# Kernel tuning notes

Hardware: AMD Instinct MI355X
Metric: run time of the kernel (lower is better)

## Reference

```python
import jax, jax.numpy as jnp
import numpy as np

GH, GW, H, B, IN = 4, 2, 512, 8192, 1
FC_HID = H // 2
NC = GH * GW
BN_EPS = 1e-5


def setup_inputs() -> dict:
    key = jax.random.key(0)
    ks = jax.random.split(key, 20)
    def n(k, shape, s=1.0):
        return jax.random.normal(k, shape, dtype=jnp.float32) * s
    return {
        "x": n(ks[0], (B, GH, GW)),
        "h_ext": n(ks[1], (B, H), 0.1),
        "c_ext": n(ks[2], (B, H), 0.1),
        "grid_h": n(ks[3], (GH, GW, B, H), 0.1),
        "grid_c": n(ks[4], (GH, GW, B, H), 0.1),
        "Wh": n(ks[5], (NC, H, 3 * H), (3 * H) ** -0.5),
        "bh": n(ks[6], (NC, H), 0.01),
        "Wc": n(ks[7], (NC, H, 3 * H), (3 * H) ** -0.5),
        "bc": n(ks[8], (NC, H), 0.01),
        "W_ih": n(ks[9], (NC, 4 * H, IN), 1.0),
        "W_hh": n(ks[10], (NC, 4 * H, H), H ** -0.5),
        "b_ih": n(ks[11], (NC, 4 * H), 0.01),
        "b_hh": n(ks[12], (NC, 4 * H), 0.01),
        "W1": n(ks[13], (FC_HID, 2 * H), (2 * H) ** -0.5),
        "b1": n(ks[14], (FC_HID,), 0.01),
        "W2": n(ks[15], (1, FC_HID), FC_HID ** -0.5),
        "b2": n(ks[16], (1,), 0.01),
        "gamma": jnp.ones((1,), jnp.float32),
        "beta": jnp.zeros((1,), jnp.float32),
    }


def _lattice_forward(x, h_ext, c_ext, grid_h, grid_c, Wh, bh, Wc, bc,
                     W_ih, W_hh, b_ih, b_hh, W1, b1, W2, b2, gamma, beta):
    b = x.shape[0]
    zeros = jnp.zeros((b, H), x.dtype)
    # python lists over the small fixed 4x2 grid (strict left/up dependency)
    sh = [[grid_h[i, j] for j in range(GW)] for i in range(GH)]
    sc = [[grid_c[i, j] for j in range(GW)] for i in range(GH)]
    for i in range(GH):
        for j in range(GW):
            k = i * GW + j
            h_prev, c_prev = sh[i][j], sc[i][j]
            if i == 0 and j == 0:
                h_left, c_left = h_ext, c_ext
            elif j > 0:
                h_left, c_left = sh[i][j - 1], sc[i][j - 1]
            else:
                h_left, c_left = zeros, zeros
            if i > 0:
                h_up, c_up = sh[i - 1][j], sc[i - 1][j]
            else:
                h_up, c_up = zeros, zeros
            comb_h = jnp.concatenate([h_left, h_up, h_prev], axis=1)  # [B,3H]
            comb_c = jnp.concatenate([c_left, c_up, c_prev], axis=1)
            ph = comb_h @ Wh[k].T + bh[k]  # [B,H]
            pc = comb_c @ Wc[k].T + bc[k]
            xi = x[:, i, j][:, None]  # [B,1]
            gates = xi @ W_ih[k].T + b_ih[k] + ph @ W_hh[k].T + b_hh[k]  # [B,4H]
            ig, fg, gg, og = jnp.split(gates, 4, axis=1)
            c_new = jax.nn.sigmoid(fg) * pc + jax.nn.sigmoid(ig) * jnp.tanh(gg)
            h_new = jax.nn.sigmoid(og) * jnp.tanh(c_new)
            sh[i][j], sc[i][j] = h_new, c_new
    final_h = sh[-1][-1] + h_ext
    final_c = sc[-1][-1] + c_ext
    final = jnp.concatenate([final_h, final_c], axis=1)  # [B,2H]
    hid = jax.nn.relu(final @ W1.T + b1)
    out = hid @ W2.T + b2  # [B,1]
    # BatchNorm1d in training mode: biased batch stats over the batch dim
    mu = jnp.mean(out, axis=0, keepdims=True)
    var = jnp.mean((out - mu) ** 2, axis=0, keepdims=True)
    out = gamma * (out - mu) * jax.lax.rsqrt(var + BN_EPS) + beta
    out = jax.nn.sigmoid(out)
    new_gh = jnp.stack([jnp.stack(row) for row in sh])  # [GH,GW,B,H]
    new_gc = jnp.stack([jnp.stack(row) for row in sc])
    return out, final_h, final_c, new_gh, new_gc


def reference(x, h_ext, c_ext, grid_h, grid_c, Wh, bh, Wc, bc,
              W_ih, W_hh, b_ih, b_hh, W1, b1, W2, b2, gamma, beta):
    return _lattice_forward(x, h_ext, c_ext, grid_h, grid_c, Wh, bh, Wc, bc,
                            W_ih, W_hh, b_ih, b_hh, W1, b1, W2, b2, gamma, beta)
```

## Files before the change

kernel.cpp:

```cpp
#include <hip/hip_runtime.h>
#include <stdint.h>

#define B_SZ 8192
#define H_SZ 512

typedef short bfrag8 __attribute__((ext_vector_type(8)));
typedef float f32x4 __attribute__((ext_vector_type(4)));

__device__ __forceinline__ unsigned short f2bf(float f) {
  union { float f; uint32_t u; } c; c.f = f;
  uint32_t u = c.u;
  uint32_t r = (u + 0x7FFFu + ((u >> 16) & 1u)) >> 16;
  return (unsigned short)r;
}
__device__ __forceinline__ float bf2f(unsigned short u) {
  union { uint32_t u; float f; } c; c.u = ((uint32_t)u) << 16;
  return c.f;
}
__device__ __forceinline__ float sigm(float x) { return 1.0f / (1.0f + __expf(-x)); }
__device__ __forceinline__ float tanh_fast(float x) {
  float cx = fminf(fmaxf(x, -15.0f), 15.0f);
  float e = __expf(2.0f * cx);
  return (e - 1.0f) / (e + 1.0f);
}

__device__ __forceinline__ void gload16(const void* g, void* l) {
  __builtin_amdgcn_global_load_lds(
      (const __attribute__((address_space(1))) void*)g,
      (__attribute__((address_space(3))) void*)l, 16, 0, 0);
}

struct GemmArgs {
  const unsigned short* Ah[3];
  const unsigned short* Ac[3];
  const unsigned short* Bh;
  const unsigned short* Bc;
  int ldA, ldB;
  const float* biash;
  const float* biasc;
  unsigned short* outBf;
  float* outF;
  const float* pc;
  const float* x;
  const float* W_ih;
  const float* b_ih;
  const float* b_hh;
  int cell, last;
  float* gh_out; float* gc_out;
  unsigned short* ring_h; unsigned short* ring_c;
  const float* h_ext; const float* c_ext;
  float* fh_out; float* fc_out;
  unsigned short* finalBf;
};

template <int MODE>
__global__ __launch_bounds__(256, 2)
void gemm_k(GemmArgs g) {
  __shared__ __align__(16) char As[16384];
  __shared__ __align__(16) char Bs[16384];
  const int tid = threadIdx.x;
  const int lane = tid & 63;
  const int wv = tid >> 6;
  const int wr = wv >> 1, wc = wv & 1;
  const int m0 = blockIdx.y * 128;
  const int z = (MODE == 0) ? blockIdx.z : 0;

  const unsigned short* const* Aseg = (MODE == 0 && z == 1) ? g.Ac : g.Ah;
  const unsigned short* Bb = (MODE == 0 && z == 1) ? g.Bc : g.Bh;

  int rowA[4], cgA[4];
  const char* browPtr[4];
#pragma unroll
  for (int q = 0; q < 4; ++q) {
    int cl = q * 256 + tid;
    int row = cl >> 3, cs = cl & 7;
    cgA[q] = cs ^ (row & 7);
    rowA[q] = row;
    int browG;
    if (MODE == 1) {
      int gate = (row >> 4) & 3;
      int hh = blockIdx.x * 32 + ((row >> 6) << 4) + (row & 15);
      browG = gate * 512 + hh;
    } else {
      browG = blockIdx.x * 128 + row;
    }
    browPtr[q] = (const char*)Bb + (size_t)browG * g.ldB * 2;
  }

  f32x4 acc[4][4];
#pragma unroll
  for (int a = 0; a < 4; ++a)
#pragma unroll
    for (int b = 0; b < 4; ++b) acc[a][b] = f32x4{0.f, 0.f, 0.f, 0.f};

  const int NSEG = (MODE == 1) ? 1 : ((MODE == 2) ? 2 : 3);
  for (int s = 0; s < NSEG; ++s) {
    const unsigned short* Ab = Aseg[s];
    if (MODE == 0 && Ab == 0) continue;
    const char* Abase = (const char*)Ab;
    const int kOffB = s * 1024;
    for (int k0 = 0; k0 < 512; k0 += 64) {
#pragma unroll
      for (int q = 0; q < 4; ++q)
        gload16(Abase + ((size_t)(m0 + rowA[q]) * g.ldA + k0) * 2 + cgA[q] * 16,
                As + (q * 256 + tid) * 16);
#pragma unroll
      for (int q = 0; q < 4; ++q)
        gload16(browPtr[q] + kOffB + k0 * 2 + cgA[q] * 16,
                Bs + (q * 256 + tid) * 16);
      __syncthreads();
#pragma unroll
      for (int ks = 0; ks < 2; ++ks) {
        bfrag8 af[4], bfr[4];
#pragma unroll
        for (int mf = 0; mf < 4; ++mf) {
          int row = wr * 64 + mf * 16 + (lane & 15);
          af[mf] = *(const bfrag8*)(As + row * 128 +
                                    ((ks * 4 + (lane >> 4)) ^ (row & 7)) * 16);
        }
#pragma unroll
        for (int nf = 0; nf < 4; ++nf) {
          int row = wc * 64 + nf * 16 + (lane & 15);
          bfr[nf] = *(const bfrag8*)(Bs + row * 128 +
                                     ((ks * 4 + (lane >> 4)) ^ (row & 7)) * 16);
        }
#pragma unroll
        for (int mf = 0; mf < 4; ++mf)
#pragma unroll
          for (int nf = 0; nf < 4; ++nf)
            acc[mf][nf] = __builtin_amdgcn_mfma_f32_16x16x32_bf16(
                af[mf], bfr[nf], acc[mf][nf], 0, 0, 0);
      }
      __syncthreads();
    }
  }

  const int c4 = lane & 15;
  const int r4 = lane >> 4;

  if (MODE == 0) {
    const float* bias = (z == 0) ? g.biash : g.biasc;
    const int n0 = blockIdx.x * 128;
#pragma unroll
    for (int nf = 0; nf < 4; ++nf) {
      int colg = n0 + wc * 64 + nf * 16 + c4;
      float bv = bias[colg];
#pragma unroll
      for (int mf = 0; mf < 4; ++mf)
#pragma unroll
        for (int r = 0; r < 4; ++r) {
          int rowg = m0 + wr * 64 + mf * 16 + r4 * 4 + r;
          float v = acc[mf][nf][r] + bv;
          if (z == 0) g.outBf[(size_t)rowg * 512 + colg] = f2bf(v);
          else        g.outF[(size_t)rowg * 512 + colg] = v;
        }
    }
  } else if (MODE == 2) {
    const int n0 = blockIdx.x * 128;
#pragma unroll
    for (int nf = 0; nf < 4; ++nf) {
      int colg = n0 + wc * 64 + nf * 16 + c4;
      float bv = g.biash[colg];
#pragma unroll
      for (int mf = 0; mf < 4; ++mf)
#pragma unroll
        for (int r = 0; r < 4; ++r) {
          int rowg = m0 + wr * 64 + mf * 16 + r4 * 4 + r;
          float v = fmaxf(acc[mf][nf][r] + bv, 0.0f);
          g.outBf[(size_t)rowg * 256 + colg] = f2bf(v);
        }
    }
  } else {
    int hcol = blockIdx.x * 32 + wc * 16 + c4;
    float wih[4], gb[4];
#pragma unroll
    for (int q = 0; q < 4; ++q) {
      wih[q] = g.W_ih[q * 512 + hcol];
      gb[q] = g.b_ih[q * 512 + hcol] + g.b_hh[q * 512 + hcol];
    }
#pragma unroll
    for (int mf = 0; mf < 4; ++mf)
#pragma unroll
      for (int r = 0; r < 4; ++r) {
        int b = m0 + wr * 64 + mf * 16 + r4 * 4 + r;
        float xi = g.x[b * 8 + g.cell];
        float vi = acc[mf][0][r] + xi * wih[0] + gb[0];
        float vf = acc[mf][1][r] + xi * wih[1] + gb[1];
        float vg = acc[mf][2][r] + xi * wih[2] + gb[2];
        float vo = acc[mf][3][r] + xi * wih[3] + gb[3];
        size_t offo = (size_t)b * 512 + hcol;
        float pcv = g.pc[offo];
        float cn = sigm(vf) * pcv + sigm(vi) * tanh_fast(vg);
        float hn = sigm(vo) * tanh_fast(cn);
        g.gh_out[offo] = hn;
        g.gc_out[offo] = cn;
        g.ring_h[offo] = f2bf(hn);
        g.ring_c[offo] = f2bf(cn);
        if (g.last) {
          float fh = hn + g.h_ext[offo];
          float fc = cn + g.c_ext[offo];
          g.fh_out[offo] = fh;
          g.fc_out[offo] = fc;
          g.finalBf[(size_t)b * 1024 + hcol] = f2bf(fh);
          g.finalBf[(size_t)b * 1024 + 512 + hcol] = f2bf(fc);
        }
      }
  }
}

__global__ __launch_bounds__(256)
void convert_pair(const float4* s0, uint2* d0, size_t n0,
                  const float4* s1, uint2* d1, size_t n1) {
  size_t total = n0 + n1;
  size_t stride = (size_t)gridDim.x * blockDim.x;
  for (size_t idx = (size_t)blockIdx.x * blockDim.x + threadIdx.x; idx < total;
       idx += stride) {
    const float4* s; uint2* d; size_t j;
    if (idx < n0) { s = s0; d = d0; j = idx; }
    else          { s = s1; d = d1; j = idx - n0; }
    float4 v = s[j];
    uint2 o;
    o.x = (uint32_t)f2bf(v.x) | ((uint32_t)f2bf(v.y) << 16);
    o.y = (uint32_t)f2bf(v.z) | ((uint32_t)f2bf(v.w) << 16);
    d[j] = o;
  }
}

__global__ __launch_bounds__(256)
void fc2_kernel(const unsigned short* hid, const float* W2, const float* b2,
                float* outlin) {
  int row = blockIdx.x * 4 + (threadIdx.x >> 6);
  int lane = threadIdx.x & 63;
  uint2 hv = ((const uint2*)(hid + (size_t)row * 256))[lane];
  float4 wv = ((const float4*)W2)[lane];
  float s = bf2f((unsigned short)(hv.x & 0xffffu)) * wv.x +
            bf2f((unsigned short)(hv.x >> 16)) * wv.y +
            bf2f((unsigned short)(hv.y & 0xffffu)) * wv.z +
            bf2f((unsigned short)(hv.y >> 16)) * wv.w;
#pragma unroll
  for (int o = 32; o > 0; o >>= 1) s += __shfl_down(s, o);
  if (lane == 0) outlin[row] = s + b2[0];
}

__global__ __launch_bounds__(1024)
void bn_kernel(const float* outlin, const float* gamma, const float* beta,
               float* out) {
  __shared__ float sred[16], sred2[16];
  __shared__ float smu, srs;
  float s = 0.f, s2 = 0.f;
  for (int i = threadIdx.x; i < 8192; i += 1024) {
    float v = outlin[i];
    s += v; s2 += v * v;
  }
#pragma unroll
  for (int o = 32; o > 0; o >>= 1) { s += __shfl_down(s, o); s2 += __shfl_down(s2, o); }
  if ((threadIdx.x & 63) == 0) { sred[threadIdx.x >> 6] = s; sred2[threadIdx.x >> 6] = s2; }
  __syncthreads();
  if (threadIdx.x == 0) {
    float S = 0.f, S2 = 0.f;
    for (int q = 0; q < 16; ++q) { S += sred[q]; S2 += sred2[q]; }
    float mu = S * (1.0f / 8192.0f);
    float var = S2 * (1.0f / 8192.0f) - mu * mu;
    smu = mu; srs = rsqrtf(var + 1e-5f);
  }
  __syncthreads();
  float gm = gamma[0], bt = beta[0];
  for (int i = threadIdx.x; i < 8192; i += 1024) {
    float v = (outlin[i] - smu) * srs * gm + bt;
    out[i] = sigm(v);
  }
}

extern "C" void kernel_launch(void* const* d_in, const int* in_sizes, int n_in,
                              void* d_out, int out_size, void* d_ws, size_t ws_size,
                              hipStream_t stream) {
  const float* x      = (const float*)d_in[0];
  const float* h_ext  = (const float*)d_in[1];
  const float* c_ext  = (const float*)d_in[2];
  const float* grid_h = (const float*)d_in[3];
  const float* grid_c = (const float*)d_in[4];
  const float* Wh     = (const float*)d_in[5];
  const float* bh     = (const float*)d_in[6];
  const float* Wc     = (const float*)d_in[7];
  const float* bc     = (const float*)d_in[8];
  const float* W_ih   = (const float*)d_in[9];
  const float* W_hh   = (const float*)d_in[10];
  const float* b_ih   = (const float*)d_in[11];
  const float* b_hh   = (const float*)d_in[12];
  const float* W1     = (const float*)d_in[13];
  const float* b1     = (const float*)d_in[14];
  const float* W2     = (const float*)d_in[15];
  const float* b2     = (const float*)d_in[16];
  const float* gamma  = (const float*)d_in[17];
  const float* beta   = (const float*)d_in[18];

  float* out = (float*)d_out;
  const size_t BH = (size_t)B_SZ * H_SZ;
  float* fh_out = out + 8192;
  float* fc_out = fh_out + BH;
  float* gh_out = fc_out + BH;
  float* gc_out = gh_out + 8 * BH;

  char* ws = (char*)d_ws;
  size_t off = 0;
  auto alloc = [&](size_t bytes) {
    char* p = ws + off;
    off = (off + bytes + 255) & ~(size_t)255;
    return p;
  };
  unsigned short* whB   = (unsigned short*)alloc(8ull * 512 * 1536 * 2);
  unsigned short* wcB   = (unsigned short*)alloc(8ull * 512 * 1536 * 2);
  unsigned short* whhB  = (unsigned short*)alloc(8ull * 2048 * 512 * 2);
  unsigned short* w1B   = (unsigned short*)alloc(256ull * 1024 * 2);
  unsigned short* hextB = (unsigned short*)alloc(BH * 2);
  unsigned short* cextB = (unsigned short*)alloc(BH * 2);
  unsigned short* ringH[3]; unsigned short* ringC[3];
  for (int s = 0; s < 3; ++s) {
    ringH[s] = (unsigned short*)alloc(BH * 2);
    ringC[s] = (unsigned short*)alloc(BH * 2);
  }
  unsigned short* phB    = (unsigned short*)alloc(BH * 2);
  float*          pcF    = (float*)alloc(BH * 4);
  unsigned short* finalB = (unsigned short*)alloc((size_t)B_SZ * 1024 * 2);
  unsigned short* hidB   = (unsigned short*)alloc((size_t)B_SZ * 256 * 2);
  float*          outlin = (float*)alloc((size_t)B_SZ * 4);

  convert_pair<<<2048, 256, 0, stream>>>((const float4*)Wh, (uint2*)whB, 8ull * 512 * 1536 / 4,
                                         (const float4*)Wc, (uint2*)wcB, 8ull * 512 * 1536 / 4);
  convert_pair<<<2048, 256, 0, stream>>>((const float4*)W_hh, (uint2*)whhB, 8ull * 2048 * 512 / 4,
                                         (const float4*)W1, (uint2*)w1B, 256ull * 1024 / 4);
  convert_pair<<<2048, 256, 0, stream>>>((const float4*)h_ext, (uint2*)hextB, BH / 4,
                                         (const float4*)c_ext, (uint2*)cextB, BH / 4);

  for (int cell = 0; cell < 8; ++cell) {
    int i = cell >> 1, j = cell & 1;
    int slot = cell % 3;
    convert_pair<<<2048, 256, 0, stream>>>(
        (const float4*)(grid_h + cell * BH), (uint2*)ringH[slot], BH / 4,
        (const float4*)(grid_c + cell * BH), (uint2*)ringC[slot], BH / 4);

    GemmArgs a = {};
    const unsigned short *hl, *cl_, *hu, *cu;
    if (cell == 0)      { hl = hextB;              cl_ = cextB; }
    else if (j > 0)     { hl = ringH[(cell - 1) % 3]; cl_ = ringC[(cell - 1) % 3]; }
    else                { hl = 0;                  cl_ = 0; }
    if (i > 0)          { hu = ringH[(cell - 2) % 3]; cu = ringC[(cell - 2) % 3]; }
    else                { hu = 0;                  cu = 0; }
    a.Ah[0] = hl; a.Ah[1] = hu; a.Ah[2] = ringH[slot];
    a.Ac[0] = cl_; a.Ac[1] = cu; a.Ac[2] = ringC[slot];
    a.Bh = whB + (size_t)cell * 512 * 1536;
    a.Bc = wcB + (size_t)cell * 512 * 1536;
    a.ldA = 512; a.ldB = 1536;
    a.biash = bh + cell * 512; a.biasc = bc + cell * 512;
    a.outBf = phB; a.outF = pcF;
    gemm_k<0><<<dim3(4, 64, 2), 256, 0, stream>>>(a);

    GemmArgs ga = {};
    ga.Ah[0] = phB; ga.ldA = 512;
    ga.Bh = whhB + (size_t)cell * 2048 * 512; ga.ldB = 512;
    ga.pc = pcF; ga.x = x;
    ga.W_ih = W_ih + cell * 2048;
    ga.b_ih = b_ih + cell * 2048;
    ga.b_hh = b_hh + cell * 2048;
    ga.cell = cell; ga.last = (cell == 7);
    ga.gh_out = gh_out + cell * BH; ga.gc_out = gc_out + cell * BH;
    ga.ring_h = ringH[slot]; ga.ring_c = ringC[slot];
    ga.h_ext = h_ext; ga.c_ext = c_ext;
    ga.fh_out = fh_out; ga.fc_out = fc_out; ga.finalBf = finalB;
    gemm_k<1><<<dim3(16, 64, 1), 256, 0, stream>>>(ga);
  }

  GemmArgs gf = {};
  gf.Ah[0] = finalB; gf.Ah[1] = finalB + 512; gf.ldA = 1024;
  gf.Bh = w1B; gf.ldB = 1024;
  gf.biash = b1;
  gf.outBf = hidB;
  gemm_k<2><<<dim3(2, 64, 1), 256, 0, stream>>>(gf);

  fc2_kernel<<<2048, 256, 0, stream>>>(hidB, W2, b2, outlin);
  bn_kernel<<<1, 1024, 0, stream>>>(outlin, gamma, beta, out);
}
```

Baseline: 786.0 us.

## Precompute h_prev/c_prev projections for all cells and batch lattice diagonals

```diff
diff --git a/kernel.cpp b/kernel.cpp
--- a/kernel.cpp
+++ b/kernel.cpp
@@ -3,6 +3,7 @@
 
 #define B_SZ 8192
 #define H_SZ 512
+static const size_t BH = (size_t)B_SZ * H_SZ;
 
 typedef short bfrag8 __attribute__((ext_vector_type(8)));
 typedef float f32x4 __attribute__((ext_vector_type(4)));
@@ -30,61 +31,40 @@
       (__attribute__((address_space(3))) void*)l, 16, 0, 0);
 }
 
-struct GemmArgs {
-  const unsigned short* Ah[3];
-  const unsigned short* Ac[3];
-  const unsigned short* Bh;
-  const unsigned short* Bc;
-  int ldA, ldB;
-  const float* biash;
-  const float* biasc;
+struct PJob {
+  const unsigned short* A0;
+  const unsigned short* A1;
+  int co0, co1, nseg, relu;
+  const unsigned short* B;
+  const float* bias;
+  const float* partial;
   unsigned short* outBf;
   float* outF;
-  const float* pc;
-  const float* x;
-  const float* W_ih;
-  const float* b_ih;
-  const float* b_hh;
-  int cell, last;
-  float* gh_out; float* gc_out;
-  unsigned short* ring_h; unsigned short* ring_c;
-  const float* h_ext; const float* c_ext;
-  float* fh_out; float* fc_out;
-  unsigned short* finalBf;
 };
-
-template <int MODE>
-__global__ __launch_bounds__(256, 2)
-void gemm_k(GemmArgs g) {
+struct PArgs {
+  PJob j[16];
+  int ldA, ldB, outStride;
+};
+
+__global__ __launch_bounds__(256, 2) void pgemm_k(PArgs pa) {
   __shared__ __align__(16) char As[16384];
   __shared__ __align__(16) char Bs[16384];
+  const PJob jb = pa.j[blockIdx.z];
   const int tid = threadIdx.x;
   const int lane = tid & 63;
   const int wv = tid >> 6;
   const int wr = wv >> 1, wc = wv & 1;
   const int m0 = blockIdx.y * 128;
-  const int z = (MODE == 0) ? blockIdx.z : 0;
-
-  const unsigned short* const* Aseg = (MODE == 0 && z == 1) ? g.Ac : g.Ah;
-  const unsigned short* Bb = (MODE == 0 && z == 1) ? g.Bc : g.Bh;
-
-  int rowA[4], cgA[4];
+
+  int rowA[4], cg[4];
   const char* browPtr[4];
 #pragma unroll
   for (int q = 0; q < 4; ++q) {
     int cl = q * 256 + tid;
     int row = cl >> 3, cs = cl & 7;
-    cgA[q] = cs ^ (row & 7);
+    cg[q] = cs ^ (row & 7);
     rowA[q] = row;
-    int browG;
-    if (MODE == 1) {
-      int gate = (row >> 4) & 3;
-      int hh = blockIdx.x * 32 + ((row >> 6) << 4) + (row & 15);
-      browG = gate * 512 + hh;
-    } else {
-      browG = blockIdx.x * 128 + row;
-    }
-    browPtr[q] = (const char*)Bb + (size_t)browG * g.ldB * 2;
+    browPtr[q] = (const char*)jb.B + (size_t)(blockIdx.x * 128 + row) * pa.ldB * 2;
   }
 
   f32x4 acc[4][4];
@@ -93,20 +73,17 @@
 #pragma unroll
     for (int b = 0; b < 4; ++b) acc[a][b] = f32x4{0.f, 0.f, 0.f, 0.f};
 
-  const int NSEG = (MODE == 1) ? 1 : ((MODE == 2) ? 2 : 3);
-  for (int s = 0; s < NSEG; ++s) {
-    const unsigned short* Ab = Aseg[s];
-    if (MODE == 0 && Ab == 0) continue;
-    const char* Abase = (const char*)Ab;
-    const int kOffB = s * 1024;
+  for (int s = 0; s < jb.nseg; ++s) {
+    const char* Abase = (const char*)(s ? jb.A1 : jb.A0);
+    const int coB = (s ? jb.co1 : jb.co0) * 2;
     for (int k0 = 0; k0 < 512; k0 += 64) {
 #pragma unroll
       for (int q = 0; q < 4; ++q)
-        gload16(Abase + ((size_t)(m0 + rowA[q]) * g.ldA + k0) * 2 + cgA[q] * 16,
+        gload16(Abase + ((size_t)(m0 + rowA[q]) * pa.ldA + k0) * 2 + cg[q] * 16,
                 As + (q * 256 + tid) * 16);
 #pragma unroll
       for (int q = 0; q < 4; ++q)
-        gload16(browPtr[q] + kOffB + k0 * 2 + cgA[q] * 16,
+        gload16(browPtr[q] + coB + k0 * 2 + cg[q] * 16,
                 Bs + (q * 256 + tid) * 16);
       __syncthreads();
 #pragma unroll
@@ -137,92 +114,166 @@
 
   const int c4 = lane & 15;
   const int r4 = lane >> 4;
-
-  if (MODE == 0) {
-    const float* bias = (z == 0) ? g.biash : g.biasc;
-    const int n0 = blockIdx.x * 128;
-#pragma unroll
-    for (int nf = 0; nf < 4; ++nf) {
-      int colg = n0 + wc * 64 + nf * 16 + c4;
-      float bv = bias[colg];
+  const int n0 = blockIdx.x * 128;
+#pragma unroll
+  for (int nf = 0; nf < 4; ++nf) {
+    int colg = n0 + wc * 64 + nf * 16 + c4;
+    float bv = jb.bias ? jb.bias[colg] : 0.0f;
+#pragma unroll
+    for (int mf = 0; mf < 4; ++mf)
+#pragma unroll
+      for (int r = 0; r < 4; ++r) {
+        int rowg = m0 + wr * 64 + mf * 16 + r4 * 4 + r;
+        size_t o = (size_t)rowg * pa.outStride + colg;
+        float v = acc[mf][nf][r] + bv;
+        if (jb.partial) v += jb.partial[o];
+        if (jb.relu) v = fmaxf(v, 0.0f);
+        if (jb.outBf) jb.outBf[o] = f2bf(v);
+        if (jb.outF) jb.outF[o] = v;
+      }
+  }
+}
+
+struct GJob {
+  const unsigned short* ph;
+  const unsigned short* Whh;
+  const float* pc;
+  float* gh; float* gc;
+  unsigned short* nh; unsigned short* nc;
+  int cell, last;
+};
+struct GArgs {
+  GJob j[2];
+  const float* x;
+  const float* W_ih; const float* b_ih; const float* b_hh;
+  const float* h_ext; const float* c_ext;
+  float* fh; float* fc;
+  unsigned short* finalB;
+};
+
+__global__ __launch_bounds__(256, 2) void gates_k(GArgs ga) {
+  __shared__ __align__(16) char As[16384];
+  __shared__ __align__(16) char Bs[16384];
+  const GJob jb = ga.j[blockIdx.z];
+  const int tid = threadIdx.x;
+  const int lane = tid & 63;
+  const int wv = tid >> 6;
+  const int wr = wv >> 1, wc = wv & 1;
+  const int m0 = blockIdx.y * 128;
+
+  int rowA[4], cg[4];
+  const char* browPtr[4];
+#pragma unroll
+  for (int q = 0; q < 4; ++q) {
+    int cl = q * 256 + tid;
+    int row = cl >> 3, cs = cl & 7;
+    cg[q] = cs ^ (row & 7);
+    rowA[q] = row;
+    int gate = (row >> 4) & 3;
+    int hh = blockIdx.x * 32 + ((row >> 6) << 4) + (row & 15);
+    browPtr[q] = (const char*)jb.Whh + (size_t)(gate * 512 + hh) * 512 * 2;
+  }
+
+  f32x4 acc[4][4];
+#pragma unroll
+  for (int a = 0; a < 4; ++a)
+#pragma unroll
+    for (int b = 0; b < 4; ++b) acc[a][b] = f32x4{0.f, 0.f, 0.f, 0.f};
+
+  for (int k0 = 0; k0 < 512; k0 += 64) {
+#pragma unroll
+    for (int q = 0; q < 4; ++q)
+      gload16((const char*)jb.ph + ((size_t)(m0 + rowA[q]) * 512 + k0) * 2 + cg[q] * 16,
+              As + (q * 256 + tid) * 16);
+#pragma unroll
+    for (int q = 0; q < 4; ++q)
+      gload16(browPtr[q] + k0 * 2 + cg[q] * 16, Bs + (q * 256 + tid) * 16);
+    __syncthreads();
+#pragma unroll
+    for (int ks = 0; ks < 2; ++ks) {
+      bfrag8 af[4], bfr[4];
+#pragma unroll
+      for (int mf = 0; mf < 4; ++mf) {
+        int row = wr * 64 + mf * 16 + (lane & 15);
+        af[mf] = *(const bfrag8*)(As + row * 128 +
+                                  ((ks * 4 + (lane >> 4)) ^ (row & 7)) * 16);
+      }
+#pragma unroll
+      for (int nf = 0; nf < 4; ++nf) {
+        int row = wc * 64 + nf * 16 + (lane & 15);
+        bfr[nf] = *(const bfrag8*)(Bs + row * 128 +
+                                   ((ks * 4 + (lane >> 4)) ^ (row & 7)) * 16);
+      }
 #pragma unroll
       for (int mf = 0; mf < 4; ++mf)
 #pragma unroll
-        for (int r = 0; r < 4; ++r) {
-          int rowg = m0 + wr * 64 + mf * 16 + r4 * 4 + r;
-          float v = acc[mf][nf][r] + bv;
-          if (z == 0) g.outBf[(size_t)rowg * 512 + colg] = f2bf(v);
-          else        g.outF[(size_t)rowg * 512 + colg] = v;
-        }
-    }
-  } else if (MODE == 2) {
-    const int n0 = blockIdx.x * 128;
-#pragma unroll
-    for (int nf = 0; nf < 4; ++nf) {
-      int colg = n0 + wc * 64 + nf * 16 + c4;
-      float bv = g.biash[colg];
-#pragma unroll
-      for (int mf = 0; mf < 4; ++mf)
-#pragma unroll
-        for (int r = 0; r < 4; ++r) {
-          int rowg = m0 + wr * 64 + mf * 16 + r4 * 4 + r;
-          float v = fmaxf(acc[mf][nf][r] + bv, 0.0f);
-          g.outBf[(size_t)rowg * 256 + colg] = f2bf(v);
-        }
-    }
-  } else {
-    int hcol = blockIdx.x * 32 + wc * 16 + c4;
-    float wih[4], gb[4];
-#pragma unroll
-    for (int q = 0; q < 4; ++q) {
-      wih[q] = g.W_ih[q * 512 + hcol];
-      gb[q] = g.b_ih[q * 512 + hcol] + g.b_hh[q * 512 + hcol];
-    }
-#pragma unroll
-    for (int mf = 0; mf < 4; ++mf)
-#pragma unroll
-      for (int r = 0; r < 4; ++r) {
-        int b = m0 + wr * 64 + mf * 16 + r4 * 4 + r;
-        float xi = g.x[b * 8 + g.cell];
-        float vi = acc[mf][0][r] + xi * wih[0] + gb[0];
-        float vf = acc[mf][1][r] + xi * wih[1] + gb[1];
-        float vg = acc[mf][2][r] + xi * wih[2] + gb[2];
-        float vo = acc[mf][3][r] + xi * wih[3] + gb[3];
-        size_t offo = (size_t)b * 512 + hcol;
-        float pcv = g.pc[offo];
-        float cn = sigm(vf) * pcv + sigm(vi) * tanh_fast(vg);
-        float hn = sigm(vo) * tanh_fast(cn);
-        g.gh_out[offo] = hn;
-        g.gc_out[offo] = cn;
-        g.ring_h[offo] = f2bf(hn);
-        g.ring_c[offo] = f2bf(cn);
-        if (g.last) {
-          float fh = hn + g.h_ext[offo];
-          float fc = cn + g.c_ext[offo];
-          g.fh_out[offo] = fh;
-          g.fc_out[offo] = fc;
-          g.finalBf[(size_t)b * 1024 + hcol] = f2bf(fh);
-          g.finalBf[(size_t)b * 1024 + 512 + hcol] = f2bf(fc);
-        }
-      }
-  }
-}
-
-__global__ __launch_bounds__(256)
-void convert_pair(const float4* s0, uint2* d0, size_t n0,
-                  const float4* s1, uint2* d1, size_t n1) {
-  size_t total = n0 + n1;
-  size_t stride = (size_t)gridDim.x * blockDim.x;
-  for (size_t idx = (size_t)blockIdx.x * blockDim.x + threadIdx.x; idx < total;
+        for (int nf = 0; nf < 4; ++nf)
+          acc[mf][nf] = __builtin_amdgcn_mfma_f32_16x16x32_bf16(
+              af[mf], bfr[nf], acc[mf][nf], 0, 0, 0);
+    }
+    __syncthreads();
+  }
+
+  const int c4 = lane & 15;
+  const int r4 = lane >> 4;
+  int hcol = blockIdx.x * 32 + wc * 16 + c4;
+  const float* Wih = ga.W_ih + jb.cell * 2048;
+  const float* bih = ga.b_ih + jb.cell * 2048;
+  const float* bhh = ga.b_hh + jb.cell * 2048;
+  float wih[4], gb[4];
+#pragma unroll
+  for (int q = 0; q < 4; ++q) {
+    wih[q] = Wih[q * 512 + hcol];
+    gb[q] = bih[q * 512 + hcol] + bhh[q * 512 + hcol];
+  }
+#pragma unroll
+  for (int mf = 0; mf < 4; ++mf)
+#pragma unroll
+    for (int r = 0; r < 4; ++r) {
+      int b = m0 + wr * 64 + mf * 16 + r4 * 4 + r;
+      float xi = ga.x[b * 8 + jb.cell];
+      float vi = acc[mf][0][r] + xi * wih[0] + gb[0];
+      float vf = acc[mf][1][r] + xi * wih[1] + gb[1];
+      float vg = acc[mf][2][r] + xi * wih[2] + gb[2];
+      float vo = acc[mf][3][r] + xi * wih[3] + gb[3];
+      size_t o = (size_t)b * 512 + hcol;
+      float pcv = jb.pc[o];
+      float cn = sigm(vf) * pcv + sigm(vi) * tanh_fast(vg);
+      float hn = sigm(vo) * tanh_fast(cn);
+      jb.gh[o] = hn;
+      jb.gc[o] = cn;
+      jb.nh[o] = f2bf(hn);
+      jb.nc[o] = f2bf(cn);
+      if (jb.last) {
+        float fh = hn + ga.h_ext[o];
+        float fc = cn + ga.c_ext[o];
+        ga.fh[o] = fh;
+        ga.fc[o] = fc;
+        ga.finalB[(size_t)b * 1024 + hcol] = f2bf(fh);
+        ga.finalB[(size_t)b * 1024 + 512 + hcol] = f2bf(fc);
+      }
+    }
+}
+
+struct CvtArgs {
+  const float4* s[8];
+  uint2* d[8];
+  long start[9];
+};
+__global__ __launch_bounds__(256) void convert_many(CvtArgs ca) {
+  long total = ca.start[8];
+  long stride = (long)gridDim.x * blockDim.x;
+  for (long idx = (long)blockIdx.x * blockDim.x + threadIdx.x; idx < total;
        idx += stride) {
-    const float4* s; uint2* d; size_t j;
-    if (idx < n0) { s = s0; d = d0; j = idx; }
-    else          { s = s1; d = d1; j = idx - n0; }
-    float4 v = s[j];
+    int jb = 0;
+#pragma unroll
+    for (int q = 1; q < 8; ++q) jb += (idx >= ca.start[q]) ? 1 : 0;
+    long local = idx - ca.start[jb];
+    float4 v = ca.s[jb][local];
     uint2 o;
     o.x = (uint32_t)f2bf(v.x) | ((uint32_t)f2bf(v.y) << 16);
     o.y = (uint32_t)f2bf(v.z) | ((uint32_t)f2bf(v.w) << 16);
-    d[j] = o;
+    ca.d[jb][local] = o;
   }
 }
 
@@ -295,7 +346,6 @@
   const float* beta   = (const float*)d_in[18];
 
   float* out = (float*)d_out;
-  const size_t BH = (size_t)B_SZ * H_SZ;
   float* fh_out = out + 8192;
   float* fc_out = fh_out + BH;
   float* gh_out = fc_out + BH;
@@ -314,68 +364,130 @@
   unsigned short* w1B   = (unsigned short*)alloc(256ull * 1024 * 2);
   unsigned short* hextB = (unsigned short*)alloc(BH * 2);
   unsigned short* cextB = (unsigned short*)alloc(BH * 2);
-  unsigned short* ringH[3]; unsigned short* ringC[3];
-  for (int s = 0; s < 3; ++s) {
-    ringH[s] = (unsigned short*)alloc(BH * 2);
-    ringC[s] = (unsigned short*)alloc(BH * 2);
-  }
-  unsigned short* phB    = (unsigned short*)alloc(BH * 2);
-  float*          pcF    = (float*)alloc(BH * 4);
+  unsigned short* prevH = (unsigned short*)alloc(8 * BH * 2);
+  unsigned short* prevC = (unsigned short*)alloc(8 * BH * 2);
+  unsigned short* newH  = (unsigned short*)alloc(8 * BH * 2);
+  unsigned short* newC  = (unsigned short*)alloc(8 * BH * 2);
+  float*          phP   = (float*)alloc(8 * BH * 4);
+  float*          pcP   = (float*)alloc(8 * BH * 4);
+  unsigned short* phB   = (unsigned short*)alloc(8 * BH * 2);
   unsigned short* finalB = (unsigned short*)alloc((size_t)B_SZ * 1024 * 2);
   unsigned short* hidB   = (unsigned short*)alloc((size_t)B_SZ * 256 * 2);
   float*          outlin = (float*)alloc((size_t)B_SZ * 4);
 
-  convert_pair<<<2048, 256, 0, stream>>>((const float4*)Wh, (uint2*)whB, 8ull * 512 * 1536 / 4,
-                                         (const float4*)Wc, (uint2*)wcB, 8ull * 512 * 1536 / 4);
-  convert_pair<<<2048, 256, 0, stream>>>((const float4*)W_hh, (uint2*)whhB, 8ull * 2048 * 512 / 4,
-                                         (const float4*)W1, (uint2*)w1B, 256ull * 1024 / 4);
-  convert_pair<<<2048, 256, 0, stream>>>((const float4*)h_ext, (uint2*)hextB, BH / 4,
-                                         (const float4*)c_ext, (uint2*)cextB, BH / 4);
-
-  for (int cell = 0; cell < 8; ++cell) {
-    int i = cell >> 1, j = cell & 1;
-    int slot = cell % 3;
-    convert_pair<<<2048, 256, 0, stream>>>(
-        (const float4*)(grid_h + cell * BH), (uint2*)ringH[slot], BH / 4,
-        (const float4*)(grid_c + cell * BH), (uint2*)ringC[slot], BH / 4);
-
-    GemmArgs a = {};
-    const unsigned short *hl, *cl_, *hu, *cu;
-    if (cell == 0)      { hl = hextB;              cl_ = cextB; }
-    else if (j > 0)     { hl = ringH[(cell - 1) % 3]; cl_ = ringC[(cell - 1) % 3]; }
-    else                { hl = 0;                  cl_ = 0; }
-    if (i > 0)          { hu = ringH[(cell - 2) % 3]; cu = ringC[(cell - 2) % 3]; }
-    else                { hu = 0;                  cu = 0; }
-    a.Ah[0] = hl; a.Ah[1] = hu; a.Ah[2] = ringH[slot];
-    a.Ac[0] = cl_; a.Ac[1] = cu; a.Ac[2] = ringC[slot];
-    a.Bh = whB + (size_t)cell * 512 * 1536;
-    a.Bc = wcB + (size_t)cell * 512 * 1536;
-    a.ldA = 512; a.ldB = 1536;
-    a.biash = bh + cell * 512; a.biasc = bc + cell * 512;
-    a.outBf = phB; a.outF = pcF;
-    gemm_k<0><<<dim3(4, 64, 2), 256, 0, stream>>>(a);
-
-    GemmArgs ga = {};
-    ga.Ah[0] = phB; ga.ldA = 512;
-    ga.Bh = whhB + (size_t)cell * 2048 * 512; ga.ldB = 512;
-    ga.pc = pcF; ga.x = x;
-    ga.W_ih = W_ih + cell * 2048;
-    ga.b_ih = b_ih + cell * 2048;
-    ga.b_hh = b_hh + cell * 2048;
-    ga.cell = cell; ga.last = (cell == 7);
-    ga.gh_out = gh_out + cell * BH; ga.gc_out = gc_out + cell * BH;
-    ga.ring_h = ringH[slot]; ga.ring_c = ringC[slot];
+  {
+    CvtArgs ca;
+    long n4[8] = {
+        8L * 512 * 1536 / 4, 8L * 512 * 1536 / 4, 8L * 2048 * 512 / 4,
+        256L * 1024 / 4,     (long)BH / 4,        (long)BH / 4,
+        8L * (long)BH / 4,   8L * (long)BH / 4};
+    const float* srcs[8] = {Wh, Wc, W_hh, W1, h_ext, c_ext, grid_h, grid_c};
+    unsigned short* dsts[8] = {whB, wcB, whhB, w1B, hextB, cextB, prevH, prevC};
+    ca.start[0] = 0;
+    for (int q = 0; q < 8; ++q) {
+      ca.s[q] = (const float4*)srcs[q];
+      ca.d[q] = (uint2*)dsts[q];
+      ca.start[q + 1] = ca.start[q] + n4[q];
+    }
+    convert_many<<<2048, 256, 0, stream>>>(ca);
+  }
+
+  {
+    PArgs pa = {};
+    pa.ldA = 512; pa.ldB = 1536; pa.outStride = 512;
+    for (int k = 0; k < 8; ++k) {
+      PJob& jh = pa.j[2 * k];
+      PJob& jc = pa.j[2 * k + 1];
+      jh = PJob{}; jc = PJob{};
+      if (k == 0) {
+        jh.A0 = hextB; jh.co0 = 0; jh.A1 = prevH; jh.co1 = 1024; jh.nseg = 2;
+        jc.A0 = cextB; jc.co0 = 0; jc.A1 = prevC; jc.co1 = 1024; jc.nseg = 2;
+        jh.outBf = phB;
+      } else {
+        jh.A0 = prevH + (size_t)k * BH; jh.co0 = 1024; jh.nseg = 1;
+        jc.A0 = prevC + (size_t)k * BH; jc.co0 = 1024; jc.nseg = 1;
+        jh.outF = phP + (size_t)k * BH;
+      }
+      jh.B = whB + (size_t)k * 512 * 1536; jh.bias = bh + k * 512;
+      jc.B = wcB + (size_t)k * 512 * 1536; jc.bias = bc + k * 512;
+      jc.outF = pcP + (size_t)k * BH;
+    }
+    pgemm_k<<<dim3(4, 64, 16), 256, 0, stream>>>(pa);
+  }
+
+  auto launch_gates = [&](const int* cells, int n) {
+    GArgs ga = {};
+    ga.x = x; ga.W_ih = W_ih; ga.b_ih = b_ih; ga.b_hh = b_hh;
     ga.h_ext = h_ext; ga.c_ext = c_ext;
-    ga.fh_out = fh_out; ga.fc_out = fc_out; ga.finalBf = finalB;
-    gemm_k<1><<<dim3(16, 64, 1), 256, 0, stream>>>(ga);
-  }
-
-  GemmArgs gf = {};
-  gf.Ah[0] = finalB; gf.Ah[1] = finalB + 512; gf.ldA = 1024;
-  gf.Bh = w1B; gf.ldB = 1024;
-  gf.biash = b1;
-  gf.outBf = hidB;
-  gemm_k<2><<<dim3(2, 64, 1), 256, 0, stream>>>(gf);
+    ga.fh = fh_out; ga.fc = fc_out; ga.finalB = finalB;
+    for (int q = 0; q < n; ++q) {
+      int k = cells[q];
+      GJob& j = ga.j[q];
+      j.ph = phB + (size_t)k * BH;
+      j.Whh = whhB + (size_t)k * 2048 * 512;
+      j.pc = pcP + (size_t)k * BH;
+      j.gh = gh_out + (size_t)k * BH;
+      j.gc = gc_out + (size_t)k * BH;
+      j.nh = newH + (size_t)k * BH;
+      j.nc = newC + (size_t)k * BH;
+      j.cell = k; j.last = (k == 7);
+    }
+    gates_k<<<dim3(16, 64, n), 256, 0, stream>>>(ga);
+  };
+
+  auto launch_serial_p = [&](const int* cells, int n) {
+    PArgs pa = {};
+    pa.ldA = 512; pa.ldB = 1536; pa.outStride = 512;
+    for (int q = 0; q < n; ++q) {
+      int k = cells[q];
+      int i = k >> 1, jj = k & 1;
+      PJob& jh = pa.j[2 * q];
+      PJob& jc = pa.j[2 * q + 1];
+      jh = PJob{}; jc = PJob{};
+      int ns = 0;
+      if (jj > 0) {
+        jh.A0 = newH + (size_t)(k - 1) * BH; jh.co0 = 0;
+        jc.A0 = newC + (size_t)(k - 1) * BH; jc.co0 = 0;
+        ns = 1;
+      }
+      if (i > 0) {
+        if (ns == 0) {
+          jh.A0 = newH + (size_t)(k - 2) * BH; jh.co0 = 512;
+          jc.A0 = newC + (size_t)(k - 2) * BH; jc.co0 = 512;
+        } else {
+          jh.A1 = newH + (size_t)(k - 2) * BH; jh.co1 = 512;
+          jc.A1 = newC + (size_t)(k - 2) * BH; jc.co1 = 512;
+        }
+        ns++;
+      }
+      jh.nseg = ns; jc.nseg = ns;
+      jh.B = whB + (size_t)k * 512 * 1536;
+      jc.B = wcB + (size_t)k * 512 * 1536;
+      jh.partial = phP + (size_t)k * BH; jh.outBf = phB + (size_t)k * BH;
+      jc.partial = pcP + (size_t)k * BH; jc.outF = pcP + (size_t)k * BH;
+    }
+    pgemm_k<<<dim3(4, 64, 2 * n), 256, 0, stream>>>(pa);
+  };
+
+  { int d0[1] = {0}; launch_gates(d0, 1); }
+  const int diags[4][2] = {{1, 2}, {3, 4}, {5, 6}, {7, -1}};
+  const int dn[4] = {2, 2, 2, 1};
+  for (int d = 0; d < 4; ++d) {
+    launch_serial_p(diags[d], dn[d]);
+    launch_gates(diags[d], dn[d]);
+  }
+
+  {
+    PArgs pa = {};
+    pa.ldA = 1024; pa.ldB = 1024; pa.outStride = 256;
+    PJob& j = pa.j[0];
+    j = PJob{};
+    j.A0 = finalB; j.co0 = 0;
+    j.A1 = finalB + 512; j.co1 = 512;
+    j.nseg = 2; j.relu = 1;
+    j.B = w1B; j.bias = b1; j.outBf = hidB;
+    pgemm_k<<<dim3(2, 64, 1), 256, 0, stream>>>(pa);
+  }
 
   fc2_kernel<<<2048, 256, 0, stream>>>(hidB, W2, b2, outlin);
   bn_kernel<<<1, 1024, 0, stream>>>(outlin, gamma, beta, out);
```

New measurement: 999.0 us. +27.1%, slower.
